# Kernel tuning notes

Hardware: AMD Instinct MI355X
Metric: run time of the kernel (lower is better)

The kernel has to match this reference:

```python
import jax, jax.numpy as jnp
import numpy as np

N_NODES = 50000
N_EDGES = 800000
IN_F = 128
OUT_F = 32
HEADS = 4
NEG_SLOPE = 0.2


def setup_inputs() -> dict:
    key = jax.random.key(0)
    ks = jax.random.split(key, 6)
    x = jax.random.normal(ks[0], (N_NODES, IN_F), dtype=jnp.float32)
    edge_index = jax.random.randint(ks[1], (2, N_EDGES), 0, N_NODES, dtype=jnp.int64)
    s = 1.0 / np.sqrt(IN_F)
    W_l = jax.random.normal(ks[2], (IN_F, HEADS * OUT_F), dtype=jnp.float32) * s
    W_r = jax.random.normal(ks[3], (IN_F, HEADS * OUT_F), dtype=jnp.float32) * s
    att = jax.random.normal(ks[4], (HEADS, OUT_F), dtype=jnp.float32) * s
    bias = jax.random.normal(ks[5], (HEADS * OUT_F,), dtype=jnp.float32) * 0.01
    return {"x": x, "edge_index": edge_index, "W_l": W_l, "W_r": W_r, "att": att, "bias": bias}


def reference(x, edge_index, W_l, W_r, att, bias):
    N = x.shape[0]
    # add self loops (PyG GATv2Conv default add_self_loops=True)
    loops = jnp.arange(N, dtype=edge_index.dtype)
    src = jnp.concatenate([edge_index[0], loops])
    dst = jnp.concatenate([edge_index[1], loops])
    # node projections: [N, H, C]
    xl = (x @ W_l).reshape(N, HEADS, OUT_F)
    xr = (x @ W_r).reshape(N, HEADS, OUT_F)
    # edge-wise GATv2 attention logits
    e = jax.nn.leaky_relu(xl[src] + xr[dst], NEG_SLOPE)  # [E, H, C]
    logits = jnp.einsum('ehc,hc->eh', e, att)  # [E, H]
    # segment softmax over destination nodes
    m = jax.ops.segment_max(logits, dst, num_segments=N)  # [N, H]
    ex = jnp.exp(logits - m[dst])
    denom = jax.ops.segment_sum(ex, dst, num_segments=N)  # [N, H]
    alpha = ex / (denom[dst] + 1e-16)  # [E, H]
    # weighted scatter-aggregate of source messages
    msg = xl[src] * alpha[:, :, None]  # [E, H, C]
    out = jax.ops.segment_sum(msg, dst, num_segments=N)  # [N, H, C]
    return out.reshape(N, HEADS * OUT_F) + bias
```

## Files before the change

kernel.cpp:

```cpp
#include <hip/hip_runtime.h>
#include <math.h>

#define IN_F 128
#define OUT_F 32
#define HEADS 4
#define HC 128
#define NEG_SLOPE 0.2f
#define LOG2E 1.44269504088896f
#define ALD 136
#define HB 256
#define BINS_U32 16384

typedef short bf16x8 __attribute__((ext_vector_type(8)));
typedef float f32x4 __attribute__((ext_vector_type(4)));

__device__ __forceinline__ unsigned short f2bf(float f) {
    unsigned u = __float_as_uint(f);
    u += 0x7FFFu + ((u >> 16) & 1u);
    return (unsigned short)(u >> 16);
}

__global__ void __launch_bounds__(512)
hist_kernel(const int* __restrict__ ei, unsigned char* __restrict__ hist,
            unsigned char* __restrict__ rank8,
            const float* __restrict__ Wl, const float* __restrict__ Wr,
            unsigned short* __restrict__ Wt, unsigned int* __restrict__ cursor,
            int N, int E0, int Etot) {
    __shared__ unsigned int h[BINS_U32];
    const int b = blockIdx.x;
    const int gt = b * 512 + threadIdx.x;
    for (int i = gt; i < 256 * IN_F; i += HB * 512) {
        const int n = i >> 7, k = i & 127;
        const float v = (n < 128) ? Wl[k * 128 + n] : Wr[k * 128 + (n - 128)];
        Wt[i] = f2bf(v);
    }
    if (gt == 0) *cursor = 0u;

    const int epb = (Etot + HB - 1) / HB;
    const int t0 = b * epb, t1 = min(t0 + epb, Etot);
    for (int i = threadIdx.x; i < BINS_U32; i += 512) h[i] = 0u;
    __syncthreads();
    for (int t = t0 + threadIdx.x; t < t1; t += 512) {
        const int dst = (t < E0) ? ei[E0 + t] : (t - E0);
        const unsigned sh = (dst & 3) * 8;
        const unsigned old = atomicAdd(&h[dst >> 2], 1u << sh);
        rank8[t] = (unsigned char)((old >> sh) & 0xFFu);
    }
    __syncthreads();
    unsigned int* row = (unsigned int*)&hist[(size_t)b * N];
    const int nw = N >> 2;
    for (int i = threadIdx.x; i < nw; i += 512) row[i] = h[i];
}

__global__ void __launch_bounds__(256)
proj_kernel(const float* __restrict__ x,
            const unsigned short* __restrict__ Wt,
            unsigned short* __restrict__ xlb,
            float* __restrict__ xr, int N) {
    __shared__ unsigned short As[64 * ALD];
    const int tid = threadIdx.x;
    const int n0 = blockIdx.x * 64;
#pragma unroll
    for (int q = 0; q < 8; ++q) {
        const int idx = q * 256 + tid;
        const int row = idx >> 5;
        const int col4 = (idx & 31) * 4;
        const float4 v = *(const float4*)&x[(size_t)min(n0 + row, N - 1) * IN_F + col4];
        ushort4 p;
        p.x = f2bf(v.x); p.y = f2bf(v.y); p.z = f2bf(v.z); p.w = f2bf(v.w);
        *(ushort4*)&As[row * ALD + col4] = p;
    }
    __syncthreads();

    const int w = tid >> 6, lane = tid & 63;
    const int lm = lane & 15, lg = lane >> 4;

    bf16x8 af[4];
#pragma unroll
    for (int kk = 0; kk < 4; ++kk)
        af[kk] = *(const bf16x8*)&As[(w * 16 + lm) * ALD + kk * 32 + lg * 8];

    f32x4 acc[16];
#pragma unroll
    for (int c = 0; c < 16; ++c) acc[c] = (f32x4){0.f, 0.f, 0.f, 0.f};

#pragma unroll
    for (int c = 0; c < 16; ++c) {
#pragma unroll
        for (int kk = 0; kk < 4; ++kk) {
            const bf16x8 bf = *(const bf16x8*)&Wt[(size_t)(c * 16 + lm) * 128 + kk * 32 + lg * 8];
            acc[c] = __builtin_amdgcn_mfma_f32_16x16x32_bf16(af[kk], bf, acc[c], 0, 0, 0);
        }
    }

    const int rbase = n0 + w * 16 + lg * 4;
#pragma unroll
    for (int c = 0; c < 16; ++c) {
#pragma unroll
        for (int r = 0; r < 4; ++r) {
            const int R = rbase + r;
            if (R >= N) continue;
            const int C = c * 16 + lm;
            if (c < 8) xlb[(size_t)R * HC + C] = f2bf(acc[c][r]);
            else       xr[(size_t)R * HC + (C - 128)] = acc[c][r];
        }
    }
}

__global__ void __launch_bounds__(64)
reduce_alloc_kernel(unsigned int* __restrict__ hist32, int* __restrict__ deg,
                    int* __restrict__ start, unsigned int* __restrict__ cursor,
                    int N4) {
    __shared__ int sc[64];
    __shared__ int base_s;
    const int tid = threadIdx.x;
    const int n4 = blockIdx.x * 64 + tid;
    int r0 = 0, r1 = 0, r2 = 0, r3 = 0;
    if (n4 < N4) {
#pragma unroll 8
        for (int b = 0; b < HB; ++b) {
            const size_t idx = (size_t)b * N4 + n4;
            const unsigned w = hist32[idx];
            hist32[idx] = (unsigned)(r0 | (r1 << 8) | (r2 << 16) | (r3 << 24));
            r0 += w & 0xFFu; r1 += (w >> 8) & 0xFFu;
            r2 += (w >> 16) & 0xFFu; r3 += (w >> 24) & 0xFFu;
        }
    }
    const int tot = r0 + r1 + r2 + r3;
    sc[tid] = tot;
    __syncthreads();
#pragma unroll
    for (int off = 1; off < 64; off <<= 1) {
        int v = (tid >= off) ? sc[tid - off] : 0;
        __syncthreads();
        sc[tid] += v;
        __syncthreads();
    }
    if (tid == 63) base_s = (int)atomicAdd(cursor, (unsigned int)sc[63]);
    __syncthreads();
    if (n4 < N4) {
        const int s = base_s + sc[tid] - tot;
        int4 st, dg;
        st.x = s; st.y = s + r0; st.z = st.y + r1; st.w = st.z + r2;
        dg.x = r0; dg.y = r1; dg.z = r2; dg.w = r3;
        *(int4*)&start[n4 * 4] = st;
        *(int4*)&deg[n4 * 4] = dg;
    }
}

__global__ void __launch_bounds__(512)
scatter2_kernel(const int* __restrict__ ei, const int* __restrict__ start,
                const unsigned char* __restrict__ hist,
                const unsigned char* __restrict__ rank8,
                int* __restrict__ esrc, int N, int E0, int Etot) {
    const int b = blockIdx.x;
    const int epb = (Etot + HB - 1) / HB;
    const int t0 = b * epb, t1 = min(t0 + epb, Etot);
    const unsigned char* hrow = &hist[(size_t)b * N];
    for (int t = t0 + threadIdx.x; t < t1; t += 512) {
        int src, dst;
        if (t < E0) { src = ei[t]; dst = ei[E0 + t]; }
        else        { src = dst = t - E0; }
        esrc[start[dst] + (int)hrow[dst] + (int)rank8[t]] = src;
    }
}

template <int CTRL>
__device__ __forceinline__ float dpp_add(float v) {
    const int t = __builtin_amdgcn_update_dpp(
        0, __float_as_int(v), CTRL, 0xF, 0xF, true);
    return v + __int_as_float(t);
}

__device__ __forceinline__ float row_sum_bcast(float c) {
    c = dpp_add<0xB1>(c);
    c = dpp_add<0x4E>(c);
    c = dpp_add<0x124>(c);
    c = dpp_add<0x128>(c);
    return c;
}

__global__ void __launch_bounds__(256)
fused_agg_kernel(const unsigned short* __restrict__ xlb,
                 const float* __restrict__ xr,
                 const float* __restrict__ att,
                 const float* __restrict__ bias,
                 const int* __restrict__ esrc,
                 const int* __restrict__ start,
                 const int* __restrict__ deg,
                 float* __restrict__ out, int N, int EtotM1) {
    const int wid = threadIdx.x >> 6;
    const int lane = threadIdx.x & 63;
    const int n = blockIdx.x * 4 + wid;
    if (n >= N) return;

    const int ch = lane * 2;
    const float2 xr2 = *(const float2*)&xr[(size_t)n * HC + ch];
    const float2 at2 = *(const float2*)&att[ch];
    const float au0 = at2.x * LOG2E, au1 = at2.y * LOG2E;
    const int s0 = start[n];
    const int d = deg[n];

    float sum = 0.f, ax = 0.f, ay = 0.f;

    auto body = [&](unsigned pk) {
        const float vx = __uint_as_float(pk << 16);
        const float vy = __uint_as_float(pk & 0xFFFF0000u);
        const float sx = vx + xr2.x;
        const float sy = vy + xr2.y;
        const float lx = fmaxf(sx, sx * NEG_SLOPE);
        const float ly = fmaxf(sy, sy * NEG_SLOPE);
        const float c = fmaf(au1, ly, au0 * lx);
        const float p = __builtin_amdgcn_exp2f(row_sum_bcast(c));
        sum += p;
        ax = fmaf(p, vx, ax);
        ay = fmaf(p, vy, ay);
    };

    for (int jb = 0; jb < d; jb += 64) {
        const int cnt = min(64, d - jb);
        const int ev = esrc[min(s0 + jb + lane, EtotM1)];

        unsigned pk0 = *(const unsigned*)&xlb[(size_t)__builtin_amdgcn_readlane(ev, 0) * HC + ch];
        unsigned pk1 = *(const unsigned*)&xlb[(size_t)__builtin_amdgcn_readlane(ev, 1) * HC + ch];
        unsigned pk2 = *(const unsigned*)&xlb[(size_t)__builtin_amdgcn_readlane(ev, 2) * HC + ch];
        unsigned pk3 = *(const unsigned*)&xlb[(size_t)__builtin_amdgcn_readlane(ev, 3) * HC + ch];

        int j = 0;
        for (; j + 3 < cnt; j += 4) {
            const unsigned q0 = *(const unsigned*)&xlb[(size_t)__builtin_amdgcn_readlane(ev, min(j + 4, 63)) * HC + ch];
            const unsigned q1 = *(const unsigned*)&xlb[(size_t)__builtin_amdgcn_readlane(ev, min(j + 5, 63)) * HC + ch];
            const unsigned q2 = *(const unsigned*)&xlb[(size_t)__builtin_amdgcn_readlane(ev, min(j + 6, 63)) * HC + ch];
            const unsigned q3 = *(const unsigned*)&xlb[(size_t)__builtin_amdgcn_readlane(ev, min(j + 7, 63)) * HC + ch];
            body(pk0); body(pk1); body(pk2); body(pk3);
            pk0 = q0; pk1 = q1; pk2 = q2; pk3 = q3;
        }
        for (; j < cnt; ++j) {
            body(pk0);
            pk0 = pk1; pk1 = pk2; pk2 = pk3;
        }
    }
    const float inv = __builtin_amdgcn_rcpf(sum + 1e-16f);
    const float2 b2 = *(const float2*)&bias[ch];
    float2 o;
    o.x = fmaf(ax, inv, b2.x);
    o.y = fmaf(ay, inv, b2.y);
    *(float2*)&out[(size_t)n * HC + ch] = o;
}

extern "C" void kernel_launch(void* const* d_in, const int* in_sizes, int n_in,
                              void* d_out, int out_size, void* d_ws, size_t ws_size,
                              hipStream_t stream) {
    const float* x    = (const float*)d_in[0];
    const int*   ei   = (const int*)d_in[1];
    const float* Wl   = (const float*)d_in[2];
    const float* Wr   = (const float*)d_in[3];
    const float* att  = (const float*)d_in[4];
    const float* bias = (const float*)d_in[5];
    float* out        = (float*)d_out;

    const int N    = in_sizes[0] / IN_F;
    const int E0   = in_sizes[1] / 2;
    const int Etot = E0 + N;

    char* base = (char*)d_ws;
    unsigned short* xlb = (unsigned short*)base; base += (size_t)N * HC * sizeof(unsigned short);
    float* xr   = (float*)base;        base += (size_t)N * HC * sizeof(float);
    int*   esrc = (int*)base;          base += (size_t)Etot * sizeof(int);
    int*   strt = (int*)base;          base += (size_t)N * sizeof(int);
    int*   deg  = (int*)base;          base += (size_t)N * sizeof(int);
    unsigned char* hist = (unsigned char*)base; base += (size_t)HB * N * sizeof(unsigned char);
    unsigned char* rank8 = (unsigned char*)base; base += (size_t)Etot * sizeof(unsigned char);
    unsigned short* Wt = (unsigned short*)base; base += 256 * IN_F * sizeof(unsigned short);
    unsigned int* cursor = (unsigned int*)base;

    hist_kernel<<<HB, 512, 0, stream>>>(ei, hist, rank8, Wl, Wr, Wt, cursor,
                                        N, E0, Etot);
    proj_kernel<<<(N + 63) / 64, 256, 0, stream>>>(x, Wt, xlb, xr, N);
    reduce_alloc_kernel<<<(N / 4 + 63) / 64, 64, 0, stream>>>(
        (unsigned int*)hist, deg, strt, cursor, N / 4);
    scatter2_kernel<<<HB, 512, 0, stream>>>(ei, strt, hist, rank8, esrc,
                                            N, E0, Etot);
    fused_agg_kernel<<<(N + 3) / 4, 256, 0, stream>>>(xlb, xr, att, bias, esrc, strt, deg,
                                                      out, N, Etot - 1);
}
```

Measured before the change: 219.1 us.

## Fuse CSR build into one cooperative kernel; deepen gather prefetch to 8

The histogram, reduce/allocate and scatter kernels are merged into one cooperative kernel that uses grid-wide syncs between phases. This removes two kernel launches and their boundaries. The reduce phase now runs as 512-thread blocks on a subset of the grid, with a wider shared-memory scan. The aggregation loop prefetches eight source rows instead of four to hide more gather latency, at the cost of extra registers. An unused dummy lambda is also added.

```diff
diff --git a/kernel.cpp b/kernel.cpp
--- a/kernel.cpp
+++ b/kernel.cpp
@@ -1,5 +1,8 @@
 #include <hip/hip_runtime.h>
+#include <hip/hip_cooperative_groups.h>
 #include <math.h>
+
+namespace cg = cooperative_groups;
 
 #define IN_F 128
 #define OUT_F 32
@@ -21,14 +24,19 @@
 }
 
 __global__ void __launch_bounds__(512)
-hist_kernel(const int* __restrict__ ei, unsigned char* __restrict__ hist,
-            unsigned char* __restrict__ rank8,
-            const float* __restrict__ Wl, const float* __restrict__ Wr,
-            unsigned short* __restrict__ Wt, unsigned int* __restrict__ cursor,
-            int N, int E0, int Etot) {
+csr_build_kernel(const int* __restrict__ ei, unsigned char* __restrict__ hist,
+                 unsigned char* __restrict__ rank8,
+                 const float* __restrict__ Wl, const float* __restrict__ Wr,
+                 unsigned short* __restrict__ Wt, unsigned int* __restrict__ cursor,
+                 int* __restrict__ deg, int* __restrict__ start,
+                 int* __restrict__ esrc, int N, int E0, int Etot) {
     __shared__ unsigned int h[BINS_U32];
+    __shared__ int base_s;
+    cg::grid_group grid = cg::this_grid();
     const int b = blockIdx.x;
-    const int gt = b * 512 + threadIdx.x;
+    const int tid = threadIdx.x;
+    const int gt = b * 512 + tid;
+
     for (int i = gt; i < 256 * IN_F; i += HB * 512) {
         const int n = i >> 7, k = i & 127;
         const float v = (n < 128) ? Wl[k * 128 + n] : Wr[k * 128 + (n - 128)];
@@ -38,18 +46,73 @@
 
     const int epb = (Etot + HB - 1) / HB;
     const int t0 = b * epb, t1 = min(t0 + epb, Etot);
-    for (int i = threadIdx.x; i < BINS_U32; i += 512) h[i] = 0u;
+    for (int i = tid; i < BINS_U32; i += 512) h[i] = 0u;
     __syncthreads();
-    for (int t = t0 + threadIdx.x; t < t1; t += 512) {
+    for (int t = t0 + tid; t < t1; t += 512) {
         const int dst = (t < E0) ? ei[E0 + t] : (t - E0);
         const unsigned sh = (dst & 3) * 8;
         const unsigned old = atomicAdd(&h[dst >> 2], 1u << sh);
         rank8[t] = (unsigned char)((old >> sh) & 0xFFu);
     }
     __syncthreads();
-    unsigned int* row = (unsigned int*)&hist[(size_t)b * N];
-    const int nw = N >> 2;
-    for (int i = threadIdx.x; i < nw; i += 512) row[i] = h[i];
+    {
+        unsigned int* row = (unsigned int*)&hist[(size_t)b * N];
+        const int nw = N >> 2;
+        for (int i = tid; i < nw; i += 512) row[i] = h[i];
+    }
+    __threadfence();
+    grid.sync();
+
+    const int N4 = N >> 2;
+    const int nbB = (N4 + 511) / 512;
+    if (b < nbB) {
+        int* sc = (int*)h;
+        unsigned int* hist32 = (unsigned int*)hist;
+        const int n4 = b * 512 + tid;
+        int r0 = 0, r1 = 0, r2 = 0, r3 = 0;
+        if (n4 < N4) {
+#pragma unroll 8
+            for (int bb = 0; bb < HB; ++bb) {
+                const size_t idx = (size_t)bb * N4 + n4;
+                const unsigned w = hist32[idx];
+                hist32[idx] = (unsigned)(r0 | (r1 << 8) | (r2 << 16) | (r3 << 24));
+                r0 += w & 0xFFu; r1 += (w >> 8) & 0xFFu;
+                r2 += (w >> 16) & 0xFFu; r3 += (w >> 24) & 0xFFu;
+            }
+        }
+        const int tot = r0 + r1 + r2 + r3;
+        sc[tid] = tot;
+        __syncthreads();
+#pragma unroll
+        for (int off = 1; off < 512; off <<= 1) {
+            int v = (tid >= off) ? sc[tid - off] : 0;
+            __syncthreads();
+            sc[tid] += v;
+            __syncthreads();
+        }
+        if (tid == 511) base_s = (int)atomicAdd(cursor, (unsigned int)sc[511]);
+        __syncthreads();
+        if (n4 < N4) {
+            const int s = base_s + sc[tid] - tot;
+            int4 st, dg;
+            st.x = s; st.y = s + r0; st.z = st.y + r1; st.w = st.z + r2;
+            dg.x = r0; dg.y = r1; dg.z = r2; dg.w = r3;
+            *(int4*)&start[n4 * 4] = st;
+            *(int4*)&deg[n4 * 4] = dg;
+        }
+    }
+    __threadfence();
+    grid.sync();
+
+    {
+        const unsigned char* hrow = &hist[(size_t)b * N];
+        for (int t = t0 + tid; t < t1; t += 512) {
+            int src, dst;
+            if (t < E0) { src = ei[t]; dst = ei[E0 + t]; }
+            else        { src = dst = t - E0; }
+            esrc[start[dst] + (int)hrow[dst] + (int)rank8[t]] = src;
+        }
+    }
 }
 
 __global__ void __launch_bounds__(256)
@@ -104,64 +167,6 @@
             if (c < 8) xlb[(size_t)R * HC + C] = f2bf(acc[c][r]);
             else       xr[(size_t)R * HC + (C - 128)] = acc[c][r];
         }
-    }
-}
-
-__global__ void __launch_bounds__(64)
-reduce_alloc_kernel(unsigned int* __restrict__ hist32, int* __restrict__ deg,
-                    int* __restrict__ start, unsigned int* __restrict__ cursor,
-                    int N4) {
-    __shared__ int sc[64];
-    __shared__ int base_s;
-    const int tid = threadIdx.x;
-    const int n4 = blockIdx.x * 64 + tid;
-    int r0 = 0, r1 = 0, r2 = 0, r3 = 0;
-    if (n4 < N4) {
-#pragma unroll 8
-        for (int b = 0; b < HB; ++b) {
-            const size_t idx = (size_t)b * N4 + n4;
-            const unsigned w = hist32[idx];
-            hist32[idx] = (unsigned)(r0 | (r1 << 8) | (r2 << 16) | (r3 << 24));
-            r0 += w & 0xFFu; r1 += (w >> 8) & 0xFFu;
-            r2 += (w >> 16) & 0xFFu; r3 += (w >> 24) & 0xFFu;
-        }
-    }
-    const int tot = r0 + r1 + r2 + r3;
-    sc[tid] = tot;
-    __syncthreads();
-#pragma unroll
-    for (int off = 1; off < 64; off <<= 1) {
-        int v = (tid >= off) ? sc[tid - off] : 0;
-        __syncthreads();
-        sc[tid] += v;
-        __syncthreads();
-    }
-    if (tid == 63) base_s = (int)atomicAdd(cursor, (unsigned int)sc[63]);
-    __syncthreads();
-    if (n4 < N4) {
-        const int s = base_s + sc[tid] - tot;
-        int4 st, dg;
-        st.x = s; st.y = s + r0; st.z = st.y + r1; st.w = st.z + r2;
-        dg.x = r0; dg.y = r1; dg.z = r2; dg.w = r3;
-        *(int4*)&start[n4 * 4] = st;
-        *(int4*)&deg[n4 * 4] = dg;
-    }
-}
-
-__global__ void __launch_bounds__(512)
-scatter2_kernel(const int* __restrict__ ei, const int* __restrict__ start,
-                const unsigned char* __restrict__ hist,
-                const unsigned char* __restrict__ rank8,
-                int* __restrict__ esrc, int N, int E0, int Etot) {
-    const int b = blockIdx.x;
-    const int epb = (Etot + HB - 1) / HB;
-    const int t0 = b * epb, t1 = min(t0 + epb, Etot);
-    const unsigned char* hrow = &hist[(size_t)b * N];
-    for (int t = t0 + threadIdx.x; t < t1; t += 512) {
-        int src, dst;
-        if (t < E0) { src = ei[t]; dst = ei[E0 + t]; }
-        else        { src = dst = t - E0; }
-        esrc[start[dst] + (int)hrow[dst] + (int)rank8[t]] = src;
     }
 }
 
@@ -217,28 +222,42 @@
         ay = fmaf(p, vy, ay);
     };
 
+    auto gat = [&](int i) -> unsigned {
+        return *(const unsigned*)&xlb[
+            (size_t)__builtin_amdgcn_readlane(0, 0) * 0 +
+            (size_t)0 + 0];
+    };
+    (void)gat;
+
     for (int jb = 0; jb < d; jb += 64) {
         const int cnt = min(64, d - jb);
         const int ev = esrc[min(s0 + jb + lane, EtotM1)];
 
-        unsigned pk0 = *(const unsigned*)&xlb[(size_t)__builtin_amdgcn_readlane(ev, 0) * HC + ch];
-        unsigned pk1 = *(const unsigned*)&xlb[(size_t)__builtin_amdgcn_readlane(ev, 1) * HC + ch];
-        unsigned pk2 = *(const unsigned*)&xlb[(size_t)__builtin_amdgcn_readlane(ev, 2) * HC + ch];
-        unsigned pk3 = *(const unsigned*)&xlb[(size_t)__builtin_amdgcn_readlane(ev, 3) * HC + ch];
+#define LDE(i) (*(const unsigned*)&xlb[(size_t)__builtin_amdgcn_readlane(ev, (i)) * HC + ch])
+        unsigned pk0 = LDE(0), pk1 = LDE(1), pk2 = LDE(2), pk3 = LDE(3);
+        unsigned pk4 = LDE(4), pk5 = LDE(5), pk6 = LDE(6), pk7 = LDE(7);
 
         int j = 0;
-        for (; j + 3 < cnt; j += 4) {
-            const unsigned q0 = *(const unsigned*)&xlb[(size_t)__builtin_amdgcn_readlane(ev, min(j + 4, 63)) * HC + ch];
-            const unsigned q1 = *(const unsigned*)&xlb[(size_t)__builtin_amdgcn_readlane(ev, min(j + 5, 63)) * HC + ch];
-            const unsigned q2 = *(const unsigned*)&xlb[(size_t)__builtin_amdgcn_readlane(ev, min(j + 6, 63)) * HC + ch];
-            const unsigned q3 = *(const unsigned*)&xlb[(size_t)__builtin_amdgcn_readlane(ev, min(j + 7, 63)) * HC + ch];
+        for (; j + 7 < cnt; j += 8) {
+            const unsigned q0 = LDE(min(j + 8, 63));
+            const unsigned q1 = LDE(min(j + 9, 63));
+            const unsigned q2 = LDE(min(j + 10, 63));
+            const unsigned q3 = LDE(min(j + 11, 63));
+            const unsigned q4 = LDE(min(j + 12, 63));
+            const unsigned q5 = LDE(min(j + 13, 63));
+            const unsigned q6 = LDE(min(j + 14, 63));
+            const unsigned q7 = LDE(min(j + 15, 63));
             body(pk0); body(pk1); body(pk2); body(pk3);
+            body(pk4); body(pk5); body(pk6); body(pk7);
             pk0 = q0; pk1 = q1; pk2 = q2; pk3 = q3;
+            pk4 = q4; pk5 = q5; pk6 = q6; pk7 = q7;
         }
         for (; j < cnt; ++j) {
             body(pk0);
-            pk0 = pk1; pk1 = pk2; pk2 = pk3;
-        }
+            pk0 = pk1; pk1 = pk2; pk2 = pk3; pk3 = pk4;
+            pk4 = pk5; pk5 = pk6; pk6 = pk7;
+        }
+#undef LDE
     }
     const float inv = __builtin_amdgcn_rcpf(sum + 1e-16f);
     const float2 b2 = *(const float2*)&bias[ch];
@@ -274,13 +293,14 @@
     unsigned short* Wt = (unsigned short*)base; base += 256 * IN_F * sizeof(unsigned short);
     unsigned int* cursor = (unsigned int*)base;
 
-    hist_kernel<<<HB, 512, 0, stream>>>(ei, hist, rank8, Wl, Wr, Wt, cursor,
-                                        N, E0, Etot);
+    int Nv = N, E0v = E0, Etotv = Etot;
+    void* cargs[] = {(void*)&ei, (void*)&hist, (void*)&rank8, (void*)&Wl, (void*)&Wr,
+                     (void*)&Wt, (void*)&cursor, (void*)&deg, (void*)&strt,
+                     (void*)&esrc, (void*)&Nv, (void*)&E0v, (void*)&Etotv};
+    hipLaunchCooperativeKernel(reinterpret_cast<void*>(csr_build_kernel),
+                               dim3(HB), dim3(512), cargs, 0, stream);
+
     proj_kernel<<<(N + 63) / 64, 256, 0, stream>>>(x, Wt, xlb, xr, N);
-    reduce_alloc_kernel<<<(N / 4 + 63) / 64, 64, 0, stream>>>(
-        (unsigned int*)hist, deg, strt, cursor, N / 4);
-    scatter2_kernel<<<HB, 512, 0, stream>>>(ei, strt, hist, rank8, esrc,
-                                            N, E0, Etot);
     fused_agg_kernel<<<(N + 3) / 4, 256, 0, stream>>>(xlb, xr, att, bias, esrc, strt, deg,
                                                       out, N, Etot - 1);
 }
```

Measured after the change: 388.9 us. +77.5%, slower.
